# Kernel tuning notes

Hardware: AMD Instinct MI355X
Metric: run time of the kernel (lower is better)

## Reference

```python
import jax, jax.numpy as jnp
import numpy as np

NH = 4  # attention heads

def rmsnorm(x, w, eps=1e-5):
    return x * jax.lax.rsqrt(jnp.mean(x * x, axis=-1, keepdims=True) + eps) * w

def gin(x, src, dst, W, b):
    # GINConv(eps=0): Linear(x + sum_{j->i} x_j)
    agg = jax.ops.segment_sum(x[src], dst, num_segments=x.shape[0])
    return (x + agg) @ W + b

def attn_pool(xb, vt, qkv_w, qkv_b, ao_w, ao_b):
    # xb: [B, Nmax, H] padded nodes (zeros participate, matching the torch code
    # which passes no key_padding_mask); vt: [T, H] virtual tokens.
    B, Nmax, H = xb.shape
    T = vt.shape[0]
    hd = H // NH
    q = (vt @ qkv_w[:, :H] + qkv_b[:H]).reshape(T, NH, hd)
    k = (xb @ qkv_w[:, H:2 * H] + qkv_b[H:2 * H]).reshape(B, Nmax, NH, hd)
    v = (xb @ qkv_w[:, 2 * H:] + qkv_b[2 * H:]).reshape(B, Nmax, NH, hd)
    scores = jnp.einsum('thd,bkhd->bhtk', q, k) / jnp.sqrt(jnp.asarray(hd, xb.dtype))
    attn = jax.nn.softmax(scores, axis=-1)
    o = jnp.einsum('bhtk,bkhd->bthd', attn, v).reshape(B, T, H)
    return o @ ao_w + ao_b

def mamba(tokens, in_w, conv_w, conv_b, x_w, dt_w, dt_b, A_log, D, out_w, norm_w, normf_w):
    # HF MambaModel with num_hidden_layers=1 (slow path), inputs_embeds path.
    B, T, H = tokens.shape
    I, K = conv_w.shape
    S = A_log.shape[1]
    R = dt_w.shape[0]
    res = tokens
    h = rmsnorm(tokens, norm_w)
    proj = h @ in_w                      # [B,T,2I]
    u, gate = jnp.split(proj, 2, axis=-1)
    up = jnp.pad(u, ((0, 0), (K - 1, 0), (0, 0)))  # causal depthwise conv1d
    conv = sum(conv_w[:, k] * up[:, k:k + T, :] for k in range(K)) + conv_b
    u = jax.nn.silu(conv)                # [B,T,I]
    ssm = u @ x_w                        # [B,T,R+2S]
    dtr, Bm, Cm = jnp.split(ssm, [R, R + S], axis=-1)
    dt = jax.nn.softplus(dtr @ dt_w + dt_b)  # [B,T,I]
    A = -jnp.exp(A_log)                  # [I,S]

    def step(hstate, inp):
        dt_t, B_t, C_t, u_t = inp        # [B,I],[B,S],[B,S],[B,I]
        dA = jnp.exp(dt_t[:, :, None] * A)
        dBu = dt_t[:, :, None] * B_t[:, None, :] * u_t[:, :, None]
        hstate = dA * hstate + dBu
        y = jnp.sum(hstate * C_t[:, None, :], axis=-1)
        return hstate, y

    h0 = jnp.zeros((B, I, S), tokens.dtype)
    xs = (dt.transpose(1, 0, 2), Bm.transpose(1, 0, 2), Cm.transpose(1, 0, 2), u.transpose(1, 0, 2))
    _, ys = jax.lax.scan(step, h0, xs)
    y = ys.transpose(1, 0, 2) + u * D
    y = y * jax.nn.silu(gate)
    out = y @ out_w                      # [B,T,H]
    return rmsnorm(res + out, normf_w)

def _forward(x, edge_index, batch, num_graphs, nodes_per_graph,
             w_in, b_in, gin_w, gin_b, vt, qkv_w, qkv_b, ao_w, ao_b,
             m_in_w, m_conv_w, m_conv_b, m_x_w, m_dt_w, m_dt_b,
             m_A_log, m_D, m_out_w, m_norm_w, m_normf_w, w_out, b_out):
    src, dst = edge_index[0], edge_index[1]
    N = x.shape[0]
    starts = jnp.searchsorted(batch, jnp.arange(num_graphs, dtype=batch.dtype))
    pos = jnp.arange(N, dtype=batch.dtype) - starts[batch]
    x = gin(x, src, dst, w_in, b_in)
    H = x.shape[-1]
    for l in range(gin_w.shape[0]):
        g = gin(x, src, dst, gin_w[l], gin_b[l])
        xb = jnp.zeros((num_graphs, nodes_per_graph, H), x.dtype).at[batch, pos].set(x)
        tokens = attn_pool(xb, vt[l], qkv_w[l], qkv_b[l], ao_w[l], ao_b[l])
        gf = mamba(tokens, m_in_w, m_conv_w, m_conv_b, m_x_w, m_dt_w, m_dt_b,
                   m_A_log, m_D, m_out_w, m_norm_w, m_normf_w)
        x = g + gf.mean(axis=1)[batch]
    x = gin(x, src, dst, w_out, b_out)
    return jax.ops.segment_sum(x, batch, num_segments=num_graphs)

def setup_inputs() -> dict:
    key = jax.random.key(0)
    ks = jax.random.split(key, 24)
    N, E, B, NPG = 131072, 2097152, 128, 1024
    IN = H = OUT = 128
    T, L = 8, 2
    I, S, R, K = 256, 16, 8, 4  # mamba: intermediate, state, dt_rank, conv kernel
    w = lambda k, s: (jax.random.normal(k, s, jnp.float32) * 0.02)
    x = jax.random.normal(ks[0], (N, IN), jnp.float32)
    edge_index = jax.random.randint(ks[1], (2, E), 0, N, jnp.int32)
    batch = (jnp.arange(N) // NPG).astype(jnp.int32)
    return dict(
        x=x, edge_index=edge_index, batch=batch, num_graphs=B, nodes_per_graph=NPG,
        w_in=w(ks[2], (IN, H)), b_in=jnp.zeros((H,), jnp.float32),
        gin_w=w(ks[3], (L, H, H)), gin_b=jnp.zeros((L, H), jnp.float32),
        vt=jax.random.normal(ks[4], (L, T, H), jnp.float32),
        qkv_w=w(ks[5], (L, H, 3 * H)), qkv_b=jnp.zeros((L, 3 * H), jnp.float32),
        ao_w=w(ks[6], (L, H, H)), ao_b=jnp.zeros((L, H), jnp.float32),
        m_in_w=w(ks[7], (H, 2 * I)),
        m_conv_w=w(ks[8], (I, K)), m_conv_b=jnp.zeros((I,), jnp.float32),
        m_x_w=w(ks[9], (I, R + 2 * S)),
        m_dt_w=w(ks[10], (R, I)), m_dt_b=jnp.full((I,), 0.1, jnp.float32),
        m_A_log=jnp.log(jnp.tile(jnp.arange(1, S + 1, dtype=jnp.float32), (I, 1))),
        m_D=jnp.ones((I,), jnp.float32),
        m_out_w=w(ks[11], (I, H)),
        m_norm_w=jnp.ones((H,), jnp.float32), m_normf_w=jnp.ones((H,), jnp.float32),
        w_out=w(ks[12], (H, OUT)), b_out=jnp.zeros((OUT,), jnp.float32),
    )

def reference(x, edge_index, batch, num_graphs, nodes_per_graph,
              w_in, b_in, gin_w, gin_b, vt, qkv_w, qkv_b, ao_w, ao_b,
              m_in_w, m_conv_w, m_conv_b, m_x_w, m_dt_w, m_dt_b,
              m_A_log, m_D, m_out_w, m_norm_w, m_normf_w, w_out, b_out):
    return _forward(x, edge_index, batch, num_graphs, nodes_per_graph,
                    w_in, b_in, gin_w, gin_b, vt, qkv_w, qkv_b, ao_w, ao_b,
                    m_in_w, m_conv_w, m_conv_b, m_x_w, m_dt_w, m_dt_b,
                    m_A_log, m_D, m_out_w, m_norm_w, m_normf_w, w_out, b_out)
```

## Files before the change

### kernel.cpp

```cpp
#include <hip/hip_runtime.h>

#define HDIM 128
#define TTOK 8
#define NPG 1024
#define NBUCK 512
#define BSHIFT 8
#define BCAP 5120
#define EPB 4096
#define PARTSZ 4160

typedef unsigned short ushort;
typedef unsigned int uint;
typedef __attribute__((ext_vector_type(8))) short short8;
typedef __attribute__((ext_vector_type(4))) float f32x4;

__device__ __forceinline__ ushort f2bf(float f) {
    unsigned int x = __float_as_uint(f);
    return (ushort)((x + 0x7FFFu + ((x >> 16) & 1u)) >> 16);
}
__device__ __forceinline__ float blo(uint u) { return __uint_as_float(u << 16); }
__device__ __forceinline__ float bhi(uint u) { return __uint_as_float(u & 0xFFFF0000u); }
__device__ __forceinline__ uint pk(float a, float b) {
    return (uint)f2bf(a) | ((uint)f2bf(b) << 16);
}

__device__ __forceinline__ void bin_body(const int* __restrict__ src,
    const int* __restrict__ dst, int mode, int* __restrict__ bcursor,
    uint* __restrict__ pairbuf, int E, int e0, int tid,
    int* lcnt, int* lbase)
{
    for (int i = tid; i < NBUCK; i += 256) lcnt[i] = 0;
    __syncthreads();
    uint pkd[16];
    int bk[16], rk[16];
    #pragma unroll
    for (int i = 0; i < 16; ++i) {
        int e = e0 + i * 256 + tid;
        int s = (e < E) ? src[e] : 0;
        int d = (e < E) ? dst[e] : 0;
        int key = mode ? s : d;
        uint pay = mode ? (uint)(d >> 10) : (uint)s;
        if (e >= E) key = -1;
        int b = key >> BSHIFT;
        bk[i] = b;
        pkd[i] = ((uint)(key & 255) << 17) | pay;
        rk[i] = (key >= 0) ? atomicAdd(&lcnt[b], 1) : 0;
    }
    __syncthreads();
    for (int i = tid; i < NBUCK; i += 256) {
        int c = lcnt[i];
        lbase[i] = c ? atomicAdd(&bcursor[i], c) : 0;
    }
    __syncthreads();
    #pragma unroll
    for (int i = 0; i < 16; ++i) {
        if (bk[i] >= 0) {
            int slot = lbase[bk[i]] + rk[i];
            if (slot < BCAP) pairbuf[(size_t)bk[i] * BCAP + slot] = pkd[i];
        }
    }
}

__global__ __launch_bounds__(256) void bin_conv_kernel(const int* __restrict__ src,
    const int* __restrict__ dst, int* __restrict__ bcursor, uint* __restrict__ pairbuf,
    int E, const float* __restrict__ xin, ushort* __restrict__ outb, int n4)
{
    __shared__ int lcnt[NBUCK];
    __shared__ int lbase[NBUCK];
    int tid = threadIdx.x;
    int b = blockIdx.x;
    if (b < NBUCK) {
        bin_body(src, dst, 0, bcursor, pairbuf, E, b * EPB, tid, lcnt, lbase);
    } else {
        for (int i = (b - NBUCK) * 256 + tid; i < n4; i += 2048 * 256) {
            float4 v = ((const float4*)xin)[i];
            uint2 o;
            o.x = pk(v.x, v.y); o.y = pk(v.z, v.w);
            ((uint2*)outb)[i] = o;
        }
    }
}

__global__ __launch_bounds__(256) void bucket_sort_kernel(const uint* __restrict__ pairbuf,
    const int* __restrict__ bcount,
    int* __restrict__ ssrc, int* __restrict__ starts, int* __restrict__ countn, int N)
{
    __shared__ int sc[NBUCK];
    __shared__ int lcount[256];
    __shared__ int lcur[256];
    __shared__ int lss[BCAP];
    int b = blockIdx.x;
    int tid = threadIdx.x;
    sc[tid] = min(bcount[tid], BCAP);
    sc[tid + 256] = min(bcount[tid + 256], BCAP);
    lcount[tid] = 0;
    __syncthreads();
    for (int off = 1; off < NBUCK; off <<= 1) {
        int a0 = (tid >= off) ? sc[tid - off] : 0;
        int a1 = (tid + 256 >= off) ? sc[tid + 256 - off] : 0;
        __syncthreads();
        sc[tid] += a0; sc[tid + 256] += a1;
        __syncthreads();
    }
    int nb = min(bcount[b], BCAP);
    int base = sc[b] - nb;
    const uint* pp = pairbuf + (size_t)b * BCAP;
    for (int i = tid; i < nb; i += 256)
        atomicAdd(&lcount[(pp[i] >> 17) & 255], 1);
    __syncthreads();
    int v = lcount[tid];
    lcur[tid] = v;
    __syncthreads();
    for (int off = 1; off < 256; off <<= 1) {
        int t = (tid >= off) ? lcur[tid - off] : 0;
        __syncthreads();
        lcur[tid] += t;
        __syncthreads();
    }
    int excl = lcur[tid] - v;
    int node = b * 256 + tid;
    starts[node] = base + excl;
    countn[node] = v;
    __syncthreads();
    lcur[tid] = excl;
    __syncthreads();
    for (int i = tid; i < nb; i += 256) {
        uint p = pp[i];
        int pos = atomicAdd(&lcur[(p >> 17) & 255], 1);
        lss[pos] = (int)(p & 0x1FFFFu);
    }
    __syncthreads();
    for (int i = tid; i < nb; i += 256) ssrc[base + i] = lss[i];
    if (b == NBUCK - 1 && tid == 0) starts[N] = base + nb;
}

__device__ __forceinline__ void gather16_body(const ushort* __restrict__ XS,
    const int* __restrict__ ssrc, const int* __restrict__ starts,
    const int* __restrict__ count, ushort* __restrict__ AGG, int nbase, int tid)
{
    int g = tid >> 4, lane = tid & 15;
    int node = nbase + g;
    uint4 sv = *((const uint4*)(XS + (size_t)node * HDIM) + lane);
    float a0 = blo(sv.x), a1 = bhi(sv.x), a2 = blo(sv.y), a3 = bhi(sv.y);
    float a4 = blo(sv.z), a5 = bhi(sv.z), a6 = blo(sv.w), a7 = bhi(sv.w);
    int s0 = starts[node], cn = count[node];
    for (int j0 = 0; j0 < cn; j0 += 16) {
        int myid = (j0 + lane < cn) ? ssrc[s0 + j0 + lane] : 0;
        int m = min(16, cn - j0);
        int j = 0;
        for (; j + 7 < m; j += 8) {
            uint4 u[8];
            #pragma unroll
            for (int q = 0; q < 8; ++q) {
                int sidx = __shfl(myid, j + q, 16);
                u[q] = *((const uint4*)(XS + (size_t)sidx * HDIM) + lane);
            }
            #pragma unroll
            for (int q = 0; q < 8; ++q) {
                a0 += blo(u[q].x); a1 += bhi(u[q].x);
                a2 += blo(u[q].y); a3 += bhi(u[q].y);
                a4 += blo(u[q].z); a5 += bhi(u[q].z);
                a6 += blo(u[q].w); a7 += bhi(u[q].w);
            }
        }
        for (; j + 3 < m; j += 4) {
            uint4 u[4];
            #pragma unroll
            for (int q = 0; q < 4; ++q) {
                int sidx = __shfl(myid, j + q, 16);
                u[q] = *((const uint4*)(XS + (size_t)sidx * HDIM) + lane);
            }
            #pragma unroll
            for (int q = 0; q < 4; ++q) {
                a0 += blo(u[q].x); a1 += bhi(u[q].x);
                a2 += blo(u[q].y); a3 += bhi(u[q].y);
                a4 += blo(u[q].z); a5 += bhi(u[q].z);
                a6 += blo(u[q].w); a7 += bhi(u[q].w);
            }
        }
        for (; j < m; ++j) {
            int sidx = __shfl(myid, j, 16);
            uint4 ua = *((const uint4*)(XS + (size_t)sidx * HDIM) + lane);
            a0 += blo(ua.x); a1 += bhi(ua.x);
            a2 += blo(ua.y); a3 += bhi(ua.y);
            a4 += blo(ua.z); a5 += bhi(ua.z);
            a6 += blo(ua.w); a7 += bhi(ua.w);
        }
    }
    uint4 o;
    o.x = pk(a0, a1); o.y = pk(a2, a3); o.z = pk(a4, a5); o.w = pk(a6, a7);
    *((uint4*)(AGG + (size_t)node * HDIM) + lane) = o;
}

__global__ __launch_bounds__(256) void gather_prep_kernel(const ushort* __restrict__ XS,
    const int* __restrict__ ssrc, const int* __restrict__ starts,
    const int* __restrict__ count, ushort* __restrict__ AGG,
    const float* __restrict__ vt, const float* __restrict__ qkv_w,
    const float* __restrict__ qkv_b, float* __restrict__ P,
    const int* __restrict__ src, const int* __restrict__ dst,
    int* __restrict__ bcursor2, uint* __restrict__ pairbuf, int E)
{
    __shared__ float vtl[TTOK][HDIM];
    __shared__ float q[TTOK][HDIM];
    __shared__ int lcnt[NBUCK];
    __shared__ int lbase[NBUCK];
    int b = blockIdx.x, tid = threadIdx.x;
    if (b < 2) {
        int l = b;
        const float* vtp = vt + (size_t)l * TTOK * HDIM;
        const float* qw = qkv_w + (size_t)l * 128 * 384;
        const float* qb = qkv_b + (size_t)l * 384;
        float* Pp = P + (size_t)l * 4 * TTOK * HDIM;
        for (int i = tid; i < TTOK * HDIM; i += 256) vtl[i >> 7][i & 127] = vtp[i];
        __syncthreads();
        for (int i = tid; i < TTOK * HDIM; i += 256) {
            int t = i >> 7, j = i & 127;
            float acc = qb[j];
            for (int c = 0; c < 128; ++c) acc += vtl[t][c] * qw[c * 384 + j];
            q[t][j] = acc;
        }
        __syncthreads();
        const float scale = 0.17677669529663687f;
        for (int i = tid; i < 4 * TTOK * HDIM; i += 256) {
            int h = i >> 10, t = (i >> 7) & 7, cc = i & 127;
            float acc = 0.f;
            for (int d = 0; d < 32; ++d)
                acc += qw[cc * 384 + 128 + h * 32 + d] * q[t][h * 32 + d];
            Pp[i] = acc * scale;
        }
    } else if (b < 8194) {
        gather16_body(XS, ssrc, starts, count, AGG, (b - 2) * 16, tid);
    } else {
        bin_body(src, dst, 1, bcursor2, pairbuf, E, (b - 8194) * EPB, tid, lcnt, lbase);
    }
}

__device__ __forceinline__ void attn_body(const ushort* __restrict__ X,
    const float* __restrict__ P, float* __restrict__ PART, int bp, int tid)
{
    __shared__ ushort Xl[64 * 128];
    __shared__ float  StU[32 * 68];
    __shared__ float lm[32], ll[32], lalpha[32];
    ushort* PlU = (ushort*)StU;
    int b = bp >> 2, part = bp & 3;
    int wave = tid >> 6, lane = tid & 63;
    int m16 = lane & 15, quad = lane >> 4;

    for (int i = tid; i < 2048; i += 256) {
        float2 v = *(const float2*)(P + (size_t)i * 2);
        ((uint*)PlU)[i] = pk(v.x, v.y);
    }
    if (tid < 32) { lm[tid] = -1e30f; ll[tid] = 0.f; }
    __syncthreads();
    short8 aP[2][4];
    #pragma unroll
    for (int mt = 0; mt < 2; ++mt)
        #pragma unroll
        for (int kc = 0; kc < 4; ++kc)
            aP[mt][kc] = *(const short8*)&PlU[(mt * 16 + m16) * 128 + (kc * 4 + quad) * 8];
    __syncthreads();

    f32x4 oacc[2][2] = {};
    const uint4* xsg = (const uint4*)(X + (size_t)b * NPG * HDIM);

    for (int tt = 0; tt < 4; ++tt) {
        {
            const uint4* xs = xsg + (part * 4 + tt) * 1024;
            uint4* xl = (uint4*)Xl;
            for (int i = tid; i < 1024; i += 256) {
                int row = i >> 4, cc = i & 15;
                xl[row * 16 + (cc ^ (row & 15))] = xs[i];
            }
        }
        __syncthreads();
        {
            f32x4 sacc[2] = {};
            #pragma unroll
            for (int kc = 0; kc < 4; ++kc) {
                int node = wave * 16 + m16;
                short8 bx = *(const short8*)&Xl[node * 128 + (((kc * 4 + quad) ^ m16) << 3)];
                sacc[0] = __builtin_amdgcn_mfma_f32_16x16x32_bf16(aP[0][kc], bx, sacc[0], 0, 0, 0);
                sacc[1] = __builtin_amdgcn_mfma_f32_16x16x32_bf16(aP[1][kc], bx, sacc[1], 0, 0, 0);
            }
            #pragma unroll
            for (int mt = 0; mt < 2; ++mt)
                #pragma unroll
                for (int r = 0; r < 4; ++r)
                    StU[(mt * 16 + quad * 4 + r) * 68 + wave * 16 + m16] = sacc[mt][r];
        }
        __syncthreads();
        {
            int j = tid >> 3, g = tid & 7;
            const float* rowp = &StU[j * 68 + g * 8];
            float4 v0 = *(const float4*)(rowp);
            float4 v1 = *(const float4*)(rowp + 4);
            float mx = fmaxf(fmaxf(fmaxf(v0.x, v0.y), fmaxf(v0.z, v0.w)),
                             fmaxf(fmaxf(v1.x, v1.y), fmaxf(v1.z, v1.w)));
            mx = fmaxf(mx, __shfl_down(mx, 4, 8));
            mx = fmaxf(mx, __shfl_down(mx, 2, 8));
            mx = fmaxf(mx, __shfl_down(mx, 1, 8));
            mx = __shfl(mx, 0, 8);
            float mold = lm[j];
            float Mn = fmaxf(mold, mx);
            float alpha = __expf(mold - Mn);
            float p0 = __expf(v0.x - Mn), p1 = __expf(v0.y - Mn);
            float p2 = __expf(v0.z - Mn), p3 = __expf(v0.w - Mn);
            float p4 = __expf(v1.x - Mn), p5 = __expf(v1.y - Mn);
            float p6 = __expf(v1.z - Mn), p7 = __expf(v1.w - Mn);
            float s = ((p0 + p1) + (p2 + p3)) + ((p4 + p5) + (p6 + p7));
            s += __shfl_down(s, 4, 8);
            s += __shfl_down(s, 2, 8);
            s += __shfl_down(s, 1, 8);
            if (g == 0) {
                ll[j] = ll[j] * alpha + s;
                lm[j] = Mn;
                lalpha[j] = alpha;
            }
            __syncthreads();
            uint4 u0;
            u0.x = pk(p0, p1); u0.y = pk(p2, p3); u0.z = pk(p4, p5); u0.w = pk(p6, p7);
            ((uint4*)PlU)[j * 8 + (g ^ (j & 7))] = u0;
        }
        __syncthreads();
        {
            #pragma unroll
            for (int mt = 0; mt < 2; ++mt)
                #pragma unroll
                for (int r = 0; r < 4; ++r) {
                    float a = lalpha[mt * 16 + quad * 4 + r];
                    oacc[mt][0][r] *= a;
                    oacc[mt][1][r] *= a;
                }
            #pragma unroll
            for (int kc = 0; kc < 2; ++kc) {
                short8 ap2[2], bx[2];
                #pragma unroll
                for (int mt = 0; mt < 2; ++mt)
                    ap2[mt] = *(const short8*)&PlU[(mt * 16 + m16) * 64
                                                   + (((kc * 4 + quad) ^ (m16 & 7)) << 3)];
                #pragma unroll
                for (int ntl = 0; ntl < 2; ++ntl) {
                    int cf = (2 * wave + ntl) * 16 + m16;
                    int chi = cf >> 3, clo = cf & 7;
                    short8 v;
                    #pragma unroll
                    for (int jj = 0; jj < 8; ++jj) {
                        int row = kc * 32 + quad * 8 + jj;
                        v[jj] = (short)Xl[(row << 7) + ((chi ^ (row & 15)) << 3) + clo];
                    }
                    bx[ntl] = v;
                }
                #pragma unroll
                for (int mt = 0; mt < 2; ++mt)
                    #pragma unroll
                    for (int ntl = 0; ntl < 2; ++ntl)
                        oacc[mt][ntl] = __builtin_amdgcn_mfma_f32_16x16x32_bf16(
                            ap2[mt], bx[ntl], oacc[mt][ntl], 0, 0, 0);
            }
        }
        __syncthreads();
    }
    float* PB = PART + ((size_t)b * 4 + part) * PARTSZ;
    #pragma unroll
    for (int mt = 0; mt < 2; ++mt)
        #pragma unroll
        for (int r = 0; r < 4; ++r) {
            int j = mt * 16 + quad * 4 + r;
            PB[j * 128 + (2 * wave + 0) * 16 + m16] = oacc[mt][0][r];
            PB[j * 128 + (2 * wave + 1) * 16 + m16] = oacc[mt][1][r];
        }
    if (tid < 32) { PB[4096 + tid] = lm[tid]; PB[4128 + tid] = ll[tid]; }
}

__global__ __launch_bounds__(256) void attn_gather_kernel(const ushort* __restrict__ X,
    const float* __restrict__ P, float* __restrict__ PART,
    const int* __restrict__ ssrc, const int* __restrict__ starts,
    const int* __restrict__ count, ushort* __restrict__ AGG)
{
    int bp = blockIdx.x;
    if (bp % 17 == 0) {
        attn_body(X, P, PART, bp / 17, threadIdx.x);
    } else {
        int gidx = bp - bp / 17 - 1;
        gather16_body(X, ssrc, starts, count, AGG, gidx * 16, threadIdx.x);
    }
}

__global__ __launch_bounds__(256) void lin128_mfma_kernel(const ushort* __restrict__ XS,
    const float* __restrict__ W, const float* __restrict__ bias,
    const float* __restrict__ GF, ushort* __restrict__ XD)
{
    __shared__ ushort Xl[128 * 128];
    __shared__ ushort Wl[128 * 128];
    int tid = threadIdx.x;
    size_t r0 = (size_t)blockIdx.x * 128;
    {
        const uint4* xs = (const uint4*)(XS + r0 * HDIM);
        uint4* xl = (uint4*)Xl;
        for (int i = tid; i < 2048; i += 256) {
            int row = i >> 4, cc = i & 15;
            xl[row * 16 + (cc ^ (row & 15))] = xs[i];
        }
    }
    {
        uint4* wl = (uint4*)Wl;
        for (int i = tid; i < 2048; i += 256) {
            int n = i & 127, c = i >> 7;
            const float* wp = W + (size_t)(c * 8) * 128 + n;
            float w0 = wp[0], w1 = wp[128], w2 = wp[256], w3 = wp[384];
            float w4 = wp[512], w5 = wp[640], w6 = wp[768], w7 = wp[896];
            uint4 u;
            u.x = pk(w0, w1); u.y = pk(w2, w3); u.z = pk(w4, w5); u.w = pk(w6, w7);
            wl[n * 16 + (c ^ (n & 15))] = u;
        }
    }
    __syncthreads();
    int wave = tid >> 6;
    int lane = tid & 63;
    int m16 = lane & 15, quad = lane >> 4;
    const short8* Xf = (const short8*)Xl;
    const short8* Wf = (const short8*)Wl;
    short8 afr[2][4];
    #pragma unroll
    for (int rt = 0; rt < 2; ++rt)
        #pragma unroll
        for (int kc = 0; kc < 4; ++kc)
            afr[rt][kc] = Xf[(wave * 32 + rt * 16 + m16) * 16 + ((kc * 4 + quad) ^ m16)];
    int graph = (int)(r0 >> 10);
    #pragma unroll
    for (int ct = 0; ct < 8; ++ct) {
        int col = ct * 16 + m16;
        short8 bfr[4];
        #pragma unroll
        for (int kc = 0; kc < 4; ++kc)
            bfr[kc] = Wf[col * 16 + ((kc * 4 + quad) ^ m16)];
        f32x4 acc0 = {0.f, 0.f, 0.f, 0.f};
        f32x4 acc1 = {0.f, 0.f, 0.f, 0.f};
        #pragma unroll
        for (int kc = 0; kc < 4; ++kc) {
            acc0 = __builtin_amdgcn_mfma_f32_16x16x32_bf16(afr[0][kc], bfr[kc], acc0, 0, 0, 0);
            acc1 = __builtin_amdgcn_mfma_f32_16x16x32_bf16(afr[1][kc], bfr[kc], acc1, 0, 0, 0);
        }
        float add = bias[col] + (GF ? GF[(size_t)graph * HDIM + col] : 0.f);
        #pragma unroll
        for (int r = 0; r < 4; ++r) {
            XD[(r0 + wave * 32 + quad * 4 + r) * HDIM + col] = f2bf(acc0[r] + add);
            XD[(r0 + wave * 32 + 16 + quad * 4 + r) * HDIM + col] = f2bf(acc1[r] + add);
        }
    }
}

__global__ __launch_bounds__(1024) void mamba_kernel(const float* __restrict__ PART,
    const float* __restrict__ qkv_w, const float* __restrict__ qkv_b,
    const float* __restrict__ ao_w, const float* __restrict__ ao_b,
    const float* __restrict__ in_w, const float* __restrict__ conv_w,
    const float* __restrict__ conv_b, const float* __restrict__ x_w,
    const float* __restrict__ dt_w, const float* __restrict__ dt_b,
    const float* __restrict__ A_log, const float* __restrict__ Dp,
    const float* __restrict__ out_w, const float* __restrict__ norm_w,
    const float* __restrict__ normf_w, float* __restrict__ GF)
{
    constexpr int I = 256, S = 16;
    __shared__ float R[32 * 132];
    __shared__ float wgt[4][32];
    __shared__ float inv[32];
    __shared__ float tok[TTOK][HDIM];
    __shared__ float hn[TTOK][HDIM];
    __shared__ float uu[TTOK][I];
    __shared__ float gg[TTOK][I];
    __shared__ float ssm[TTOK][40];
    __shared__ float yy[TTOK][I];
    int b = blockIdx.x, tid = threadIdx.x;

    const float* PB = PART + (size_t)b * 4 * PARTSZ;
    if (tid < 32) {
        int j = tid;
        float m0 = PB[4096 + j], m1 = PB[PARTSZ + 4096 + j];
        float m2 = PB[2 * PARTSZ + 4096 + j], m3 = PB[3 * PARTSZ + 4096 + j];
        float M = fmaxf(fmaxf(m0, m1), fmaxf(m2, m3));
        float w0 = __expf(m0 - M), w1 = __expf(m1 - M);
        float w2 = __expf(m2 - M), w3 = __expf(m3 - M);
        float L = w0 * PB[4128 + j] + w1 * PB[PARTSZ + 4128 + j]
                + w2 * PB[2 * PARTSZ + 4128 + j] + w3 * PB[3 * PARTSZ + 4128 + j];
        wgt[0][j] = w0; wgt[1][j] = w1; wgt[2][j] = w2; wgt[3][j] = w3;
        inv[j] = 1.f / L;
    }
    __syncthreads();
    #pragma unroll
    for (int it = 0; it < 4; ++it) {
        int idx = it * 1024 + tid;
        int j = idx >> 7, c = idx & 127;
        float v = wgt[0][j] * PB[idx] + wgt[1][j] * PB[PARTSZ + idx]
                + wgt[2][j] * PB[2 * PARTSZ + idx] + wgt[3][j] * PB[3 * PARTSZ + idx];
        R[j * 132 + c] = v * inv[j];
    }
    __syncthreads();
    {
        int t = tid >> 7, col = tid & 127;
        int h = col >> 5;
        const float* rp = &R[(h * 8 + t) * 132];
        const float* wp = qkv_w + 256 + col;
        float acc = qkv_b[256 + col];
        for (int c = 0; c < 128; c += 8) {
            float w[8];
            #pragma unroll
            for (int q = 0; q < 8; ++q) w[q] = wp[(size_t)(c + q) * 384];
            #pragma unroll
            for (int q = 0; q < 8; ++q) acc += rp[c + q] * w[q];
        }
        hn[t][col] = acc;
    }
    __syncthreads();
    {
        int t = tid >> 7, col = tid & 127;
        const float* hp = hn[t];
        const float* wp = ao_w + col;
        float acc = ao_b[col];
        for (int k = 0; k < 128; k += 8) {
            float w[8];
            #pragma unroll
            for (int q = 0; q < 8; ++q) w[q] = wp[(size_t)(k + q) * 128];
            #pragma unroll
            for (int q = 0; q < 8; ++q) acc += hp[k + q] * w[q];
        }
        tok[t][col] = acc;
    }
    __syncthreads();

    if (tid < 512) {
        int t = tid >> 6, lane = tid & 63;
        float v0 = tok[t][lane], v1 = tok[t][lane + 64];
        float s = v0 * v0 + v1 * v1;
        #pragma unroll
        for (int off = 32; off; off >>= 1) s += __shfl_down(s, off);
        s = __shfl(s, 0);
        float r = rsqrtf(s * (1.f / 128.f) + 1e-5f);
        hn[t][lane] = v0 * r * norm_w[lane];
        hn[t][lane + 64] = v1 * r * norm_w[lane + 64];
    }
    __syncthreads();
    {
        int j = tid & 511, tq = tid >> 9;
        float acc[4] = {0.f, 0.f, 0.f, 0.f};
        const float* wp = in_w + j;
        for (int c = 0; c < 128; c += 8) {
            float w[8];
            #pragma unroll
            for (int q = 0; q < 8; ++q) w[q] = wp[(size_t)(c + q) * 512];
            #pragma unroll
            for (int q = 0; q < 8; ++q) {
                float wq = w[q];
                #pragma unroll
                for (int k = 0; k < 4; ++k) acc[k] += hn[tq * 4 + k][c + q] * wq;
            }
        }
        if (j < 256) {
            #pragma unroll
            for (int k = 0; k < 4; ++k) uu[tq * 4 + k][j] = acc[k];
        } else {
            #pragma unroll
            for (int k = 0; k < 4; ++k) gg[tq * 4 + k][j - 256] = acc[k];
        }
    }
    __syncthreads();
    if (tid < 256) {
        int i = tid;
        float cw0 = conv_w[i * 4 + 0], cw1 = conv_w[i * 4 + 1];
        float cw2 = conv_w[i * 4 + 2], cw3 = conv_w[i * 4 + 3];
        float cb = conv_b[i];
        float uv[TTOK];
        #pragma unroll
        for (int t = 0; t < TTOK; ++t) uv[t] = uu[t][i];
        #pragma unroll
        for (int t = 0; t < TTOK; ++t) {
            float a = cw3 * uv[t] + cb;
            if (t >= 1) a += cw2 * uv[t - 1];
            if (t >= 2) a += cw1 * uv[t - 2];
            if (t >= 3) a += cw0 * uv[t - 3];
            float sg = 1.f / (1.f + __expf(-a));
            uu[t][i] = a * sg;
        }
    }
    __syncthreads();
    {
        int t = tid >> 7, j = tid & 127;
        if (j < 40) {
            float acc = 0.f;
            const float* wp = x_w + j;
            const float* up = uu[t];
            for (int c = 0; c < 256; c += 8) {
                float w[8];
                #pragma unroll
                for (int q = 0; q < 8; ++q) w[q] = wp[(size_t)(c + q) * 40];
                #pragma unroll
                for (int q = 0; q < 8; ++q) acc += up[c + q] * w[q];
            }
            ssm[t][j] = acc;
        }
    }
    __syncthreads();
    if (tid < 256) {
        int i = tid;
        float dw[8];
        #pragma unroll
        for (int r = 0; r < 8; ++r) dw[r] = dt_w[r * 256 + i];
        float dtbias = dt_b[i];
        float a[S], st[S];
        #pragma unroll
        for (int s = 0; s < S; ++s) { a[s] = -__expf(A_log[i * S + s]); st[s] = 0.f; }
        float Di = Dp[i];
        for (int t = 0; t < TTOK; ++t) {
            float d = dtbias;
            #pragma unroll
            for (int r = 0; r < 8; ++r) d += ssm[t][r] * dw[r];
            d = (d > 20.f) ? d : log1pf(__expf(d));
            float ut = uu[t][i];
            float du = d * ut;
            float y = 0.f;
            #pragma unroll
            for (int s = 0; s < S; ++s) {
                float dA = __expf(d * a[s]);
                st[s] = dA * st[s] + du * ssm[t][8 + s];
                y += st[s] * ssm[t][24 + s];
            }
            y += ut * Di;
            float g = gg[t][i];
            float sg = 1.f / (1.f + __expf(-g));
            yy[t][i] = y * g * sg;
        }
    }
    __syncthreads();
    {
        int t = tid >> 7, c = tid & 127;
        float acc = tok[t][c];
        const float* wp = out_w + c;
        const float* yp = yy[t];
        for (int i = 0; i < 256; i += 8) {
            float w[8];
            #pragma unroll
            for (int q = 0; q < 8; ++q) w[q] = wp[(size_t)(i + q) * 128];
            #pragma unroll
            for (int q = 0; q < 8; ++q) acc += yp[i + q] * w[q];
        }
        hn[t][c] = acc;
    }
    __syncthreads();
    if (tid < 512) {
        int t = tid >> 6, lane = tid & 63;
        float v0 = hn[t][lane], v1 = hn[t][lane + 64];
        float s = v0 * v0 + v1 * v1;
        #pragma unroll
        for (int off = 32; off; off >>= 1) s += __shfl_down(s, off);
        s = __shfl(s, 0);
        float r = rsqrtf(s * (1.f / 128.f) + 1e-5f);
        hn[t][lane] = v0 * r * normf_w[lane];
        hn[t][lane + 64] = v1 * r * normf_w[lane + 64];
    }
    __syncthreads();
    if (tid < 128) {
        float s = 0.f;
        #pragma unroll
        for (int t = 0; t < TTOK; ++t) s += hn[t][tid];
        GF[(size_t)b * HDIM + tid] = s * (1.f / TTOK);
    }
}

__global__ __launch_bounds__(512) void final_count_kernel(const ushort* __restrict__ X,
    const uint* __restrict__ pairbuf, const int* __restrict__ bcount,
    float* __restrict__ PS2)
{
    __shared__ uint hist[128 * 66];
    __shared__ ushort Xb[128 * 128];
    int bkt = blockIdx.x, tid = threadIdx.x;
    for (int i = tid; i < 128 * 66; i += 512) hist[i] = 0u;
    __syncthreads();
    int nb = min(bcount[bkt], BCAP);
    const uint* pp = pairbuf + (size_t)bkt * BCAP;
    for (int i = tid; i < nb; i += 512) {
        uint p = pp[i];
        int g = (int)(p & 0x1FFFFu);
        int s = (int)((p >> 17) & 255);
        atomicAdd(&hist[g * 66 + (s >> 2)], 1u << ((s & 3) * 8));
    }
    if (tid < 256) {
        int g = bkt >> 2;
        atomicAdd(&hist[g * 66 + (tid >> 2)], 1u << ((tid & 3) * 8));
    }
    int wave = tid >> 6, lane = tid & 63;
    int m16 = lane & 15, quad = lane >> 4;
    int grow = wave * 16 + m16;
    f32x4 acc[8] = {};
    for (int half = 0; half < 2; ++half) {
        __syncthreads();
        {
            const uint4* xs = (const uint4*)(X + ((size_t)bkt * 256 + half * 128) * HDIM);
            uint4* xl = (uint4*)Xb;
            for (int i = tid; i < 2048; i += 512) {
                int row = i >> 4, cc = i & 15;
                xl[row * 16 + (cc ^ (row & 15))] = xs[i];
            }
        }
        __syncthreads();
        #pragma unroll
        for (int kc = 0; kc < 4; ++kc) {
            int s0 = half * 128 + kc * 32 + quad * 8;
            uint w0 = hist[grow * 66 + (s0 >> 2)];
            uint w1 = hist[grow * 66 + (s0 >> 2) + 1];
            short8 afr;
            ((uint*)&afr)[0] = pk((float)(w0 & 255u), (float)((w0 >> 8) & 255u));
            ((uint*)&afr)[1] = pk((float)((w0 >> 16) & 255u), (float)(w0 >> 24));
            ((uint*)&afr)[2] = pk((float)(w1 & 255u), (float)((w1 >> 8) & 255u));
            ((uint*)&afr)[3] = pk((float)((w1 >> 16) & 255u), (float)(w1 >> 24));
            #pragma unroll
            for (int ct = 0; ct < 8; ++ct) {
                int n = ct * 16 + m16;
                int chi = n >> 3, clo = n & 7;
                short8 bx;
                #pragma unroll
                for (int j = 0; j < 8; ++j) {
                    int k = kc * 32 + quad * 8 + j;
                    bx[j] = (short)Xb[(k << 7) + ((chi ^ (k & 15)) << 3) + clo];
                }
                acc[ct] = __builtin_amdgcn_mfma_f32_16x16x32_bf16(afr, bx, acc[ct], 0, 0, 0);
            }
        }
    }
    #pragma unroll
    for (int ct = 0; ct < 8; ++ct) {
        int n = ct * 16 + m16;
        #pragma unroll
        for (int r = 0; r < 4; ++r)
            PS2[(size_t)(wave * 16 + quad * 4 + r) * (NBUCK * 128)
                + (size_t)bkt * 128 + n] = acc[ct][r];
    }
}

__global__ __launch_bounds__(512) void final_mm_kernel(const float* __restrict__ PS2,
    const float* __restrict__ w_out, const float* __restrict__ b_out,
    float* __restrict__ out)
{
    __shared__ float red[4][128];
    __shared__ float Sm[HDIM];
    int b = blockIdx.x, tid = threadIdx.x;
    int c = tid & 127, q = tid >> 7;
    const float* base = PS2 + (size_t)b * (NBUCK * 128) + c;
    float s0 = 0.f, s1 = 0.f, s2 = 0.f, s3 = 0.f;
    int k0 = q * 128;
    for (int k = k0; k < k0 + 128; k += 4) {
        s0 += base[(size_t)(k + 0) * 128];
        s1 += base[(size_t)(k + 1) * 128];
        s2 += base[(size_t)(k + 2) * 128];
        s3 += base[(size_t)(k + 3) * 128];
    }
    red[q][c] = (s0 + s1) + (s2 + s3);
    __syncthreads();
    if (tid < 128) {
        Sm[tid] = (red[0][tid] + red[1][tid]) + (red[2][tid] + red[3][tid]);
    }
    __syncthreads();
    if (tid < 128) {
        float acc = 1024.f * b_out[tid];
        for (int k = 0; k < 128; ++k) acc += Sm[k] * w_out[k * 128 + tid];
        out[(size_t)b * HDIM + tid] = acc;
    }
}

extern "C" void kernel_launch(void* const* d_in, const int* in_sizes, int n_in,
                              void* d_out, int out_size, void* d_ws, size_t ws_size,
                              hipStream_t stream)
{
    const int N = in_sizes[0] / HDIM;
    const int E = in_sizes[1] / 2;
    const int B = N >> 10;

    const float* x_in  = (const float*)d_in[0];
    const int*   src   = (const int*)d_in[1];
    const int*   dst   = src + E;
    const float* w_in  = (const float*)d_in[5];
    const float* b_in  = (const float*)d_in[6];
    const float* gin_w = (const float*)d_in[7];
    const float* gin_b = (const float*)d_in[8];
    const float* vt    = (const float*)d_in[9];
    const float* qkv_w = (const float*)d_in[10];
    const float* qkv_b = (const float*)d_in[11];
    const float* ao_w  = (const float*)d_in[12];
    const float* ao_b  = (const float*)d_in[13];
    const float* m_in_w   = (const float*)d_in[14];
    const float* m_conv_w = (const float*)d_in[15];
    const float* m_conv_b = (const float*)d_in[16];
    const float* m_x_w    = (const float*)d_in[17];
    const float* m_dt_w   = (const float*)d_in[18];
    const float* m_dt_b   = (const float*)d_in[19];
    const float* m_A_log  = (const float*)d_in[20];
    const float* m_D      = (const float*)d_in[21];
    const float* m_out_w  = (const float*)d_in[22];
    const float* m_norm_w = (const float*)d_in[23];
    const float* m_normf_w= (const float*)d_in[24];
    const float* w_out = (const float*)d_in[25];
    const float* b_out = (const float*)d_in[26];
    float* out = (float*)d_out;

    float* GF  = (float*)d_ws;
    float* P   = GF + (size_t)B * HDIM;
    float* PART= P + 2 * 4 * TTOK * HDIM;
    int* bcursor  = (int*)(PART + (size_t)B * 4 * PARTSZ);
    int* bcursor2 = bcursor + NBUCK;
    int* count    = bcursor2 + NBUCK;
    int* starts   = count + N;
    int* ssrc     = starts + N + 8;
    uint* pairbuf = (uint*)(ssrc + E);
    float* PS2    = (float*)(pairbuf + (size_t)NBUCK * BCAP);
    ushort* AGG = (ushort*)PS2;
    ushort* XB0 = (ushort*)(PS2 + (size_t)NBUCK * 128 * 128);
    ushort* XB1 = XB0 + (size_t)N * HDIM;

    const int NBB = (E + EPB - 1) / EPB;

    hipMemsetAsync(bcursor, 0, 2 * NBUCK * sizeof(int), stream);
    bin_conv_kernel<<<NBB + 2048, 256, 0, stream>>>(src, dst, bcursor, pairbuf, E,
                                                    x_in, XB0, N * 32);
    bucket_sort_kernel<<<NBUCK, 256, 0, stream>>>(pairbuf, bcursor, ssrc, starts, count, N);

    gather_prep_kernel<<<2 + N / 16 + NBB, 256, 0, stream>>>(XB0, ssrc, starts, count, AGG,
                                                             vt, qkv_w, qkv_b, P,
                                                             src, dst, bcursor2, pairbuf, E);
    lin128_mfma_kernel<<<N / 128, 256, 0, stream>>>(AGG, w_in, b_in, nullptr, XB1);

    ushort* Xcur = XB1;
    ushort* Xnext = XB0;
    const int nAG = B * 4 + N / 16;
    for (int l = 0; l < 2; ++l) {
        attn_gather_kernel<<<nAG, 256, 0, stream>>>(Xcur, P + (size_t)l * 4 * TTOK * HDIM,
                                                    PART, ssrc, starts, count, AGG);
        mamba_kernel<<<B, 1024, 0, stream>>>(PART,
                                             qkv_w + (size_t)l * 128 * 384,
                                             qkv_b + (size_t)l * 384,
                                             ao_w + (size_t)l * 128 * 128,
                                             ao_b + (size_t)l * 128,
                                             m_in_w, m_conv_w, m_conv_b, m_x_w,
                                             m_dt_w, m_dt_b, m_A_log, m_D, m_out_w,
                                             m_norm_w, m_normf_w, GF);
        lin128_mfma_kernel<<<N / 128, 256, 0, stream>>>(AGG, gin_w + (size_t)l * 128 * 128,
                                                        gin_b + (size_t)l * 128, GF, Xnext);
        ushort* t = Xcur; Xcur = Xnext; Xnext = t;
    }

    final_count_kernel<<<NBUCK, 512, 0, stream>>>(Xcur, pairbuf, bcursor2, PS2);
    final_mm_kernel<<<B, 512, 0, stream>>>(PS2, w_out, b_out, out);

    (void)n_in; (void)out_size; (void)ws_size;
}
```

Before: 793.3 us.

## Stage binned edges in shared memory and move second binning into first kernel

New measurement: 786.2 us. About the same (-0.9%).

```diff
diff --git a/kernel.cpp b/kernel.cpp
--- a/kernel.cpp
+++ b/kernel.cpp
@@ -24,55 +24,72 @@
     return (uint)f2bf(a) | ((uint)f2bf(b) << 16);
 }
 
-__device__ __forceinline__ void bin_body(const int* __restrict__ src,
-    const int* __restrict__ dst, int mode, int* __restrict__ bcursor,
-    uint* __restrict__ pairbuf, int E, int e0, int tid,
-    int* lcnt, int* lbase)
-{
-    for (int i = tid; i < NBUCK; i += 256) lcnt[i] = 0;
-    __syncthreads();
-    uint pkd[16];
-    int bk[16], rk[16];
-    #pragma unroll
-    for (int i = 0; i < 16; ++i) {
-        int e = e0 + i * 256 + tid;
-        int s = (e < E) ? src[e] : 0;
-        int d = (e < E) ? dst[e] : 0;
-        int key = mode ? s : d;
-        uint pay = mode ? (uint)(d >> 10) : (uint)s;
-        if (e >= E) key = -1;
-        int b = key >> BSHIFT;
-        bk[i] = b;
-        pkd[i] = ((uint)(key & 255) << 17) | pay;
-        rk[i] = (key >= 0) ? atomicAdd(&lcnt[b], 1) : 0;
-    }
-    __syncthreads();
-    for (int i = tid; i < NBUCK; i += 256) {
-        int c = lcnt[i];
-        lbase[i] = c ? atomicAdd(&bcursor[i], c) : 0;
-    }
-    __syncthreads();
-    #pragma unroll
-    for (int i = 0; i < 16; ++i) {
-        if (bk[i] >= 0) {
-            int slot = lbase[bk[i]] + rk[i];
-            if (slot < BCAP) pairbuf[(size_t)bk[i] * BCAP + slot] = pkd[i];
-        }
-    }
-}
-
 __global__ __launch_bounds__(256) void bin_conv_kernel(const int* __restrict__ src,
     const int* __restrict__ dst, int* __restrict__ bcursor, uint* __restrict__ pairbuf,
-    int E, const float* __restrict__ xin, ushort* __restrict__ outb, int n4)
+    int* __restrict__ bcursor2, uint* __restrict__ pairbuf2, int E,
+    const float* __restrict__ xin, ushort* __restrict__ outb, int n4)
 {
     __shared__ int lcnt[NBUCK];
-    __shared__ int lbase[NBUCK];
-    int tid = threadIdx.x;
-    int b = blockIdx.x;
-    if (b < NBUCK) {
-        bin_body(src, dst, 0, bcursor, pairbuf, E, b * EPB, tid, lcnt, lbase);
+    __shared__ int lexcl[NBUCK];
+    __shared__ int gbase[NBUCK];
+    __shared__ uint lsorted[EPB];
+    __shared__ ushort lbkt[EPB];
+    int tid = threadIdx.x, b = blockIdx.x;
+    if (b < 2 * NBUCK) {
+        int mode = (b >= NBUCK) ? 1 : 0;
+        int e0 = (mode ? b - NBUCK : b) * EPB;
+        int* bc = mode ? bcursor2 : bcursor;
+        uint* pb = mode ? pairbuf2 : pairbuf;
+        for (int i = tid; i < NBUCK; i += 256) lcnt[i] = 0;
+        __syncthreads();
+        uint pkd[16];
+        int bk[16], rk[16];
+        #pragma unroll
+        for (int i = 0; i < 16; ++i) {
+            int e = e0 + i * 256 + tid;
+            int s = (e < E) ? src[e] : 0;
+            int d = (e < E) ? dst[e] : 0;
+            int key = mode ? s : d;
+            uint pay = mode ? (uint)(d >> 10) : (uint)s;
+            if (e >= E) key = -1;
+            int bb = key >> BSHIFT;
+            bk[i] = bb;
+            pkd[i] = ((uint)(key & 255) << 17) | pay;
+            rk[i] = (key >= 0) ? atomicAdd(&lcnt[bb], 1) : 0;
+        }
+        __syncthreads();
+        lexcl[tid] = lcnt[tid];
+        lexcl[tid + 256] = lcnt[tid + 256];
+        __syncthreads();
+        for (int off = 1; off < NBUCK; off <<= 1) {
+            int a0 = (tid >= off) ? lexcl[tid - off] : 0;
+            int a1 = (tid + 256 >= off) ? lexcl[tid + 256 - off] : 0;
+            __syncthreads();
+            lexcl[tid] += a0; lexcl[tid + 256] += a1;
+            __syncthreads();
+        }
+        for (int i = tid; i < NBUCK; i += 256) {
+            int c = lcnt[i];
+            gbase[i] = c ? atomicAdd(&bc[i], c) : 0;
+        }
+        __syncthreads();
+        #pragma unroll
+        for (int i = 0; i < 16; ++i) {
+            if (bk[i] >= 0) {
+                int pos = lexcl[bk[i]] - lcnt[bk[i]] + rk[i];
+                lsorted[pos] = pkd[i];
+                lbkt[pos] = (ushort)bk[i];
+            }
+        }
+        __syncthreads();
+        int total = lexcl[NBUCK - 1];
+        for (int i = tid; i < total; i += 256) {
+            int bb = lbkt[i];
+            int slot = gbase[bb] + (i - (lexcl[bb] - lcnt[bb]));
+            if (slot < BCAP) pb[(size_t)bb * BCAP + slot] = lsorted[i];
+        }
     } else {
-        for (int i = (b - NBUCK) * 256 + tid; i < n4; i += 2048 * 256) {
+        for (int i = (b - 2 * NBUCK) * 256 + tid; i < n4; i += 2048 * 256) {
             float4 v = ((const float4*)xin)[i];
             uint2 o;
             o.x = pk(v.x, v.y); o.y = pk(v.z, v.w);
@@ -196,14 +213,10 @@
     const int* __restrict__ ssrc, const int* __restrict__ starts,
     const int* __restrict__ count, ushort* __restrict__ AGG,
     const float* __restrict__ vt, const float* __restrict__ qkv_w,
-    const float* __restrict__ qkv_b, float* __restrict__ P,
-    const int* __restrict__ src, const int* __restrict__ dst,
-    int* __restrict__ bcursor2, uint* __restrict__ pairbuf, int E)
+    const float* __restrict__ qkv_b, float* __restrict__ P)
 {
     __shared__ float vtl[TTOK][HDIM];
     __shared__ float q[TTOK][HDIM];
-    __shared__ int lcnt[NBUCK];
-    __shared__ int lbase[NBUCK];
     int b = blockIdx.x, tid = threadIdx.x;
     if (b < 2) {
         int l = b;
@@ -228,10 +241,8 @@
                 acc += qw[cc * 384 + 128 + h * 32 + d] * q[t][h * 32 + d];
             Pp[i] = acc * scale;
         }
-    } else if (b < 8194) {
+    } else {
         gather16_body(XS, ssrc, starts, count, AGG, (b - 2) * 16, tid);
-    } else {
-        bin_body(src, dst, 1, bcursor2, pairbuf, E, (b - 8194) * EPB, tid, lcnt, lbase);
     }
 }
 
@@ -808,22 +819,21 @@
     int* count    = bcursor2 + NBUCK;
     int* starts   = count + N;
     int* ssrc     = starts + N + 8;
-    uint* pairbuf = (uint*)(ssrc + E);
-    float* PS2    = (float*)(pairbuf + (size_t)NBUCK * BCAP);
+    uint* pairbuf  = (uint*)(ssrc + E);
+    uint* pairbuf2 = pairbuf + (size_t)NBUCK * BCAP;
+    float* PS2    = (float*)(pairbuf2 + (size_t)NBUCK * BCAP);
     ushort* AGG = (ushort*)PS2;
     ushort* XB0 = (ushort*)(PS2 + (size_t)NBUCK * 128 * 128);
     ushort* XB1 = XB0 + (size_t)N * HDIM;
 
-    const int NBB = (E + EPB - 1) / EPB;
-
     hipMemsetAsync(bcursor, 0, 2 * NBUCK * sizeof(int), stream);
-    bin_conv_kernel<<<NBB + 2048, 256, 0, stream>>>(src, dst, bcursor, pairbuf, E,
-                                                    x_in, XB0, N * 32);
+    bin_conv_kernel<<<2 * NBUCK + 2048, 256, 0, stream>>>(src, dst, bcursor, pairbuf,
+                                                          bcursor2, pairbuf2, E,
+                                                          x_in, XB0, N * 32);
     bucket_sort_kernel<<<NBUCK, 256, 0, stream>>>(pairbuf, bcursor, ssrc, starts, count, N);
 
-    gather_prep_kernel<<<2 + N / 16 + NBB, 256, 0, stream>>>(XB0, ssrc, starts, count, AGG,
-                                                             vt, qkv_w, qkv_b, P,
-                                                             src, dst, bcursor2, pairbuf, E);
+    gather_prep_kernel<<<2 + N / 16, 256, 0, stream>>>(XB0, ssrc, starts, count, AGG,
+                                                       vt, qkv_w, qkv_b, P);
     lin128_mfma_kernel<<<N / 128, 256, 0, stream>>>(AGG, w_in, b_in, nullptr, XB1);
 
     ushort* Xcur = XB1;
@@ -845,7 +855,7 @@
         ushort* t = Xcur; Xcur = Xnext; Xnext = t;
     }
 
-    final_count_kernel<<<NBUCK, 512, 0, stream>>>(Xcur, pairbuf, bcursor2, PS2);
+    final_count_kernel<<<NBUCK, 512, 0, stream>>>(Xcur, pairbuf2, bcursor2, PS2);
     final_mm_kernel<<<B, 512, 0, stream>>>(PS2, w_out, b_out, out);
 
     (void)n_in; (void)out_size; (void)ws_size;
```
